# Kernel tuning notes

Hardware: AMD Instinct MI355X
Metric: run time of the kernel (lower is better)

The kernel has to match this reference:

```python
import jax, jax.numpy as jnp
import numpy as np

N_HEADS = 32
N_KV_HEADS = 8
HEAD_DIM = 128
GROUP = N_HEADS // N_KV_HEADS  # 4
MAX_SEQ_LEN = 4096
DIM = 3072
NEG_BIG = 1.0e9


def setup_inputs() -> dict:
    key = jax.random.key(0)
    ks = jax.random.split(key, 8)
    B, T = 1, 2048
    return {
        "x": jax.random.normal(ks[0], (B, T, DIM), dtype=jnp.float32),
        "freqs_cos": jax.random.uniform(ks[1], (T, HEAD_DIM // 2), dtype=jnp.float32),
        "freqs_sin": jax.random.uniform(ks[2], (T, HEAD_DIM // 2), dtype=jnp.float32),
        "input_pos": jnp.arange(T, dtype=jnp.int32),
        "wq": jax.random.normal(ks[3], (N_HEADS * HEAD_DIM, DIM), dtype=jnp.float32) * 0.02,
        "wk": jax.random.normal(ks[4], (N_KV_HEADS * HEAD_DIM, DIM), dtype=jnp.float32) * 0.02,
        "wv": jax.random.normal(ks[5], (N_KV_HEADS * HEAD_DIM, DIM), dtype=jnp.float32) * 0.02,
        "wo": jax.random.normal(ks[6], (DIM, N_HEADS * HEAD_DIM), dtype=jnp.float32) * 0.02,
        "k_cache": jnp.zeros((1, N_KV_HEADS, MAX_SEQ_LEN, HEAD_DIM), dtype=jnp.float32),
        "v_cache": jnp.zeros((1, N_KV_HEADS, MAX_SEQ_LEN, HEAD_DIM), dtype=jnp.float32),
    }


def _rotate_half(x):
    half = x.shape[-1] // 2
    return jnp.concatenate([-x[..., half:], x[..., :half]], axis=-1)


def _apply_rope(q, k, freqs_cos, freqs_sin):
    # freqs: [T, D/2] -> [1, T, 1, D] (tiled x2, matching torch repeat on last dim)
    fc = jnp.concatenate([freqs_cos, freqs_cos], axis=-1)[None, :, None, :]
    fs = jnp.concatenate([freqs_sin, freqs_sin], axis=-1)[None, :, None, :]
    qf = q.astype(jnp.float32)
    kf = k.astype(jnp.float32)
    q_out = qf * fc + _rotate_half(qf) * fs
    k_out = kf * fc + _rotate_half(kf) * fs
    return q_out.astype(q.dtype), k_out.astype(k.dtype)


def reference(x, freqs_cos, freqs_sin, input_pos, wq, wk, wv, wo, k_cache, v_cache):
    B, T, _ = x.shape
    # QKV projections
    q = (x @ wq.T).reshape(B, T, N_HEADS, HEAD_DIM)
    k = (x @ wk.T).reshape(B, T, N_KV_HEADS, HEAD_DIM)
    v = (x @ wv.T).reshape(B, T, N_KV_HEADS, HEAD_DIM)
    # split-half RoPE (computed in fp32)
    q, k = _apply_rope(q, k, freqs_cos, freqs_sin)
    # StaticKVCache.update: scatter [B,H,T,D] into [1,H,S,D] cache at input_pos (dim 2)
    kc = k_cache.at[:, :, input_pos].set(k.transpose(0, 2, 1, 3))
    vc = v_cache.at[:, :, input_pos].set(v.transpose(0, 2, 1, 3))
    # MetalSDPA: additive causal mask over full cache length
    S = kc.shape[2]
    k_pos = jnp.arange(S)
    valid = jnp.clip(input_pos[:, None] - k_pos[None, :] + 1, 0, 1)  # [T, S]
    mask = (valid.astype(q.dtype) - 1.0) * NEG_BIG
    # GQA attention: group q heads per kv head
    qg = q.transpose(0, 2, 1, 3).reshape(B, N_KV_HEADS, GROUP, T, HEAD_DIM)
    scale = 1.0 / jnp.sqrt(jnp.asarray(HEAD_DIM, dtype=q.dtype))
    scores = jnp.einsum('bhgtd,bhsd->bhgts', qg, kc) * scale + mask  # [B,Hk,G,T,S]
    attn = jax.nn.softmax(scores, axis=-1)
    y = jnp.einsum('bhgts,bhsd->bhgtd', attn, vc)
    y = y.reshape(B, N_HEADS, T, HEAD_DIM).transpose(0, 2, 1, 3).reshape(B, T, N_HEADS * HEAD_DIM)
    return y @ wo.T
```

## Files before the change

kernel.cpp:

```cpp
#include <hip/hip_runtime.h>

typedef __attribute__((ext_vector_type(8))) short bf16x8;
typedef __attribute__((ext_vector_type(4))) float f32x4;

#define T_SEQ   2048
#define DIM     3072
#define NQH     32
#define NKVH    8
#define HD      128
#define QDIM    4096
#define KVDIM   1024
#define QKVDIM  6144

#define AS1 __attribute__((address_space(1)))
#define AS3 __attribute__((address_space(3)))

static __device__ __forceinline__ unsigned short f2bf(float f) {
  unsigned u = __float_as_uint(f);
  u += 0x7FFFu + ((u >> 16) & 1u);
  return (unsigned short)(u >> 16);
}
static __device__ __forceinline__ float bf2f(unsigned short h) {
  return __uint_as_float(((unsigned)h) << 16);
}

static __device__ __forceinline__ void gload_lds16(const unsigned short* g, unsigned short* l) {
  __builtin_amdgcn_global_load_lds((AS1 void*)(g), (AS3 void*)(l), 16, 0, 0);
}

__global__ void cvt_f32_bf16(const float* __restrict__ src, unsigned short* __restrict__ dst, int n4) {
  int i = blockIdx.x * blockDim.x + threadIdx.x;
  if (i >= n4) return;
  float4 v = reinterpret_cast<const float4*>(src)[i];
  ushort4 o;
  o.x = f2bf(v.x); o.y = f2bf(v.y); o.z = f2bf(v.z); o.w = f2bf(v.w);
  reinterpret_cast<ushort4*>(dst)[i] = o;
}

template<int OUTBF>
__global__ __launch_bounds__(256) void gemm_bt(
    const unsigned short* __restrict__ A, const unsigned short* __restrict__ B,
    float* __restrict__ Cf, unsigned short* __restrict__ Cb,
    int M, int N, int K) {
  __shared__ unsigned short la[128 * 64];
  __shared__ unsigned short lb[128 * 64];
  const int nbx = N >> 7;
  const int q8 = gridDim.x >> 3;
  int bid = blockIdx.x;
  bid = (bid & 7) * q8 + (bid >> 3);
  const int bx = bid % nbx, by = bid / nbx;
  const int tid = threadIdx.x;
  const int ln = tid & 63;
  const int wave = tid >> 6;
  const int lr = ln & 15, lg = ln >> 4;
  const int wr = wave >> 1, wc = wave & 1;
  const int rowA0 = by << 7, rowB0 = bx << 7;

  f32x4 acc[4][4] = {};

  const int ktn = K >> 6;
  for (int kt = 0; kt < ktn; kt++) {
    __syncthreads();
#pragma unroll
    for (int it = 0; it < 4; it++) {
      int ci = it * 256 + tid;
      int r = ci >> 3, cpos = ci & 7;
      int c = cpos ^ (r & 7);
      const unsigned short* gA = A + (size_t)(rowA0 + r) * K + kt * 64 + c * 8;
      const unsigned short* gB = B + (size_t)(rowB0 + r) * K + kt * 64 + c * 8;
      gload_lds16(gA, &la[ci * 8]);
      gload_lds16(gB, &lb[ci * 8]);
    }
    __syncthreads();
#pragma unroll
    for (int kk = 0; kk < 2; kk++) {
      bf16x8 af[4], bfr[4];
#pragma unroll
      for (int mi = 0; mi < 4; mi++) {
        int r = wr * 64 + mi * 16 + lr;
        int p = (kk * 4 + lg) ^ (r & 7);
        af[mi] = *reinterpret_cast<const bf16x8*>(&la[r * 64 + p * 8]);
      }
#pragma unroll
      for (int ni = 0; ni < 4; ni++) {
        int r = wc * 64 + ni * 16 + lr;
        int p = (kk * 4 + lg) ^ (r & 7);
        bfr[ni] = *reinterpret_cast<const bf16x8*>(&lb[r * 64 + p * 8]);
      }
#pragma unroll
      for (int mi = 0; mi < 4; mi++)
#pragma unroll
        for (int ni = 0; ni < 4; ni++)
          acc[mi][ni] = __builtin_amdgcn_mfma_f32_16x16x32_bf16(af[mi], bfr[ni], acc[mi][ni], 0, 0, 0);
    }
  }
#pragma unroll
  for (int mi = 0; mi < 4; mi++)
#pragma unroll
    for (int ni = 0; ni < 4; ni++)
#pragma unroll
      for (int j = 0; j < 4; j++) {
        int r = rowA0 + wr * 64 + mi * 16 + lg * 4 + j;
        int cc = rowB0 + wc * 64 + ni * 16 + lr;
        if (OUTBF) Cb[(size_t)r * N + cc] = f2bf(acc[mi][ni][j]);
        else       Cf[(size_t)r * N + cc] = acc[mi][ni][j];
      }
}

__global__ void rope_repack(const unsigned short* __restrict__ qkv,
                            const float* __restrict__ fc, const float* __restrict__ fs,
                            unsigned short* __restrict__ qo, unsigned short* __restrict__ ko) {
  int idx = blockIdx.x * blockDim.x + threadIdx.x;
  int d = idx & 63;
  int hh = (idx >> 6) % 40;
  int t = idx / 2560;
  const unsigned short* src = qkv + (size_t)t * QKVDIM + hh * 128;
  float x0 = bf2f(src[d]);
  float x1 = bf2f(src[d + 64]);
  float c = fc[t * 64 + d], s = fs[t * 64 + d];
  float o0 = x0 * c - x1 * s;
  float o1 = x1 * c + x0 * s;
  if (hh < 32) {
    unsigned short* dst = qo + (size_t)t * QDIM + hh * 128;
    dst[d] = f2bf(o0); dst[d + 64] = f2bf(o1);
  } else {
    unsigned short* dst = ko + (size_t)t * KVDIM + (hh - 32) * 128;
    dst[d] = f2bf(o0); dst[d + 64] = f2bf(o1);
  }
}

__global__ void vtrans(const unsigned short* __restrict__ qkv, unsigned short* __restrict__ vt) {
  __shared__ unsigned short tile[64][68];
  int tb = blockIdx.x * 64, cb = blockIdx.y * 64;
  int tid = threadIdx.x;
#pragma unroll
  for (int i = 0; i < 16; i++) {
    int e = i * 256 + tid;
    int tl = e >> 6, cl = e & 63;
    tile[tl][cl] = qkv[(size_t)(tb + tl) * QKVDIM + 5120 + cb + cl];
  }
  __syncthreads();
#pragma unroll
  for (int i = 0; i < 16; i++) {
    int e = i * 256 + tid;
    int cl = e >> 6, tl = e & 63;
    vt[(size_t)(cb + cl) * T_SEQ + tb + tl] = tile[tl][cl];
  }
}

__global__ __launch_bounds__(256) void attn_fwd(
    const unsigned short* __restrict__ q, const unsigned short* __restrict__ k,
    const unsigned short* __restrict__ vt, unsigned short* __restrict__ y) {
  __shared__ unsigned short k_lds[32 * 128];
  __shared__ unsigned short v_lds[128 * 32];
  __shared__ unsigned short p_lds[4][16 * 40];
  __shared__ float a_lds[4][16];
  const int tid = threadIdx.x;
  const int ln = tid & 63;
  const int wave = tid >> 6;
  const int lr = ln & 15, lg = ln >> 4;

  const int kh = blockIdx.x & 7;
  const int i = blockIdx.x >> 3;
  const int qh = i & 3;
  const int j = i >> 2;
  const int qt = (j & 1) ? (31 - (j >> 1)) : (j >> 1);
  const int h = kh * 4 + qh;

  const int qr0 = qt * 64 + wave * 16;
  const int qrow = qr0 + lr;
  const float SL2E = 0.08838834764831845f * 1.44269504088896f;
  const float NEGINF = -__builtin_inff();

  bf16x8 qf[4];
  const unsigned short* qb = q + (size_t)qrow * QDIM + h * HD + lg * 8;
#pragma unroll
  for (int dc = 0; dc < 4; dc++) qf[dc] = *reinterpret_cast<const bf16x8*>(qb + dc * 32);

  f32x4 acc[8] = {};
  float m = NEGINF, lsum = 0.f;

  const int ntiles = (qt * 64 + 95) >> 5;
  for (int st = 0; st < ntiles; st++) {
    const int sb = st * 32;

    bf16x8 kr[2], vr[2];
#pragma unroll
    for (int it = 0; it < 2; it++) {
      int id = tid + it * 256;
      int r = id >> 4, c = id & 15;
      kr[it] = *reinterpret_cast<const bf16x8*>(k + (size_t)(sb + r) * KVDIM + kh * HD + c * 8);
      int d = id >> 2, cv = id & 3;
      vr[it] = *reinterpret_cast<const bf16x8*>(vt + (size_t)(kh * HD + d) * T_SEQ + sb + cv * 8);
    }
    __syncthreads();
#pragma unroll
    for (int it = 0; it < 2; it++) {
      int id = tid + it * 256;
      int r = id >> 4, c = id & 15;
      *reinterpret_cast<bf16x8*>(&k_lds[r * 128 + (c ^ (r & 7)) * 8]) = kr[it];
      int d = id >> 2, cv = id & 3;
      *reinterpret_cast<bf16x8*>(&v_lds[d * 32 + (cv ^ ((d >> 1) & 3)) * 8]) = vr[it];
    }
    __syncthreads();

    if (sb <= qr0 + 15) {
      f32x4 s0t = {0.f, 0.f, 0.f, 0.f}, s1t = {0.f, 0.f, 0.f, 0.f};
#pragma unroll
      for (int dc = 0; dc < 4; dc++) {
        int c = lg + dc * 4;
        int p = c ^ (lr & 7);
        bf16x8 a0 = *reinterpret_cast<const bf16x8*>(&k_lds[lr * 128 + p * 8]);
        bf16x8 a1 = *reinterpret_cast<const bf16x8*>(&k_lds[(lr + 16) * 128 + p * 8]);
        s0t = __builtin_amdgcn_mfma_f32_16x16x32_bf16(a0, qf[dc], s0t, 0, 0, 0);
        s1t = __builtin_amdgcn_mfma_f32_16x16x32_bf16(a1, qf[dc], s1t, 0, 0, 0);
      }

      float vv[8];
      if (sb + 31 <= qr0) {
#pragma unroll
        for (int jj = 0; jj < 4; jj++) { vv[jj] = s0t[jj]; vv[jj + 4] = s1t[jj]; }
      } else {
        const int base0 = sb + lg * 4;
#pragma unroll
        for (int jj = 0; jj < 4; jj++) {
          vv[jj]     = (base0 + jj      <= qrow) ? s0t[jj] : NEGINF;
          vv[jj + 4] = (base0 + jj + 16 <= qrow) ? s1t[jj] : NEGINF;
        }
      }

      float mx = fmaxf(fmaxf(fmaxf(vv[0], vv[1]), fmaxf(vv[2], vv[3])),
                       fmaxf(fmaxf(vv[4], vv[5]), fmaxf(vv[6], vv[7])));
      mx = fmaxf(mx, __shfl_xor(mx, 16));
      mx = fmaxf(mx, __shfl_xor(mx, 32));

      const bool doresc = __any(mx > m + 60.0f);
      const float mn = doresc ? fmaxf(m, mx) : m;

      float p[8], ps = 0.f;
#pragma unroll
      for (int ii = 0; ii < 8; ii++) { p[ii] = exp2f((vv[ii] - mn) * SL2E); ps += p[ii]; }
      ps += __shfl_xor(ps, 16);
      ps += __shfl_xor(ps, 32);

      ushort4 pw0, pw1;
      pw0.x = f2bf(p[0]); pw0.y = f2bf(p[1]); pw0.z = f2bf(p[2]); pw0.w = f2bf(p[3]);
      pw1.x = f2bf(p[4]); pw1.y = f2bf(p[5]); pw1.z = f2bf(p[6]); pw1.w = f2bf(p[7]);
      *reinterpret_cast<ushort4*>(&p_lds[wave][lr * 40 + lg * 4])      = pw0;
      *reinterpret_cast<ushort4*>(&p_lds[wave][lr * 40 + 16 + lg * 4]) = pw1;

      if (doresc) {
        const float alpha = exp2f((m - mn) * SL2E);
        lsum = lsum * alpha + ps;
        m = mn;
        a_lds[wave][lr] = alpha;
        asm volatile("s_waitcnt lgkmcnt(0)" ::: "memory");
        float4 a4 = *reinterpret_cast<const float4*>(&a_lds[wave][lg * 4]);
#pragma unroll
        for (int dc2 = 0; dc2 < 8; dc2++) {
          acc[dc2][0] *= a4.x; acc[dc2][1] *= a4.y;
          acc[dc2][2] *= a4.z; acc[dc2][3] *= a4.w;
        }
      } else {
        lsum += ps;
        asm volatile("s_waitcnt lgkmcnt(0)" ::: "memory");
      }

      bf16x8 pa = *reinterpret_cast<const bf16x8*>(&p_lds[wave][lr * 40 + lg * 8]);
#pragma unroll
      for (int dc2 = 0; dc2 < 8; dc2++) {
        int d = dc2 * 16 + lr;
        int p2 = lg ^ ((d >> 1) & 3);
        bf16x8 bv = *reinterpret_cast<const bf16x8*>(&v_lds[d * 32 + p2 * 8]);
        acc[dc2] = __builtin_amdgcn_mfma_f32_16x16x32_bf16(pa, bv, acc[dc2], 0, 0, 0);
      }
    }
  }

  a_lds[wave][lr] = 1.0f / lsum;
  asm volatile("s_waitcnt lgkmcnt(0)" ::: "memory");
  float4 l4 = *reinterpret_cast<const float4*>(&a_lds[wave][lg * 4]);
  float li[4] = {l4.x, l4.y, l4.z, l4.w};
#pragma unroll
  for (int jj = 0; jj < 4; jj++) {
    int r = qr0 + lg * 4 + jj;
#pragma unroll
    for (int dc2 = 0; dc2 < 8; dc2++)
      y[(size_t)r * QDIM + h * HD + dc2 * 16 + lr] = f2bf(acc[dc2][jj] * li[jj]);
  }
}

extern "C" void kernel_launch(void* const* d_in, const int* in_sizes, int n_in,
                              void* d_out, int out_size, void* d_ws, size_t ws_size,
                              hipStream_t stream) {
  (void)in_sizes; (void)n_in; (void)out_size; (void)ws_size;
  const float* x    = (const float*)d_in[0];
  const float* fcos = (const float*)d_in[1];
  const float* fsin = (const float*)d_in[2];
  const float* wq   = (const float*)d_in[4];
  const float* wk   = (const float*)d_in[5];
  const float* wv   = (const float*)d_in[6];
  const float* wo   = (const float*)d_in[7];
  float* out = (float*)d_out;
  char* ws = (char*)d_ws;

  unsigned short* x_bf    = (unsigned short*)(ws);
  unsigned short* wqkv_bf = (unsigned short*)(ws + 12582912);
  unsigned short* qkv_bf  = (unsigned short*)(ws + 50331648);
  unsigned short* q_bf    = (unsigned short*)(ws);
  unsigned short* k_bf    = (unsigned short*)(ws + 16777216);
  unsigned short* vt_bf   = (unsigned short*)(ws + 20971520);
  unsigned short* y_bf    = (unsigned short*)(ws + 25165824);
  unsigned short* wo_bf   = (unsigned short*)(ws + 50331648);

  cvt_f32_bf16<<<6144,  256, 0, stream>>>(x,  x_bf,               2048 * 3072 / 4);
  cvt_f32_bf16<<<12288, 256, 0, stream>>>(wq, wqkv_bf,            4096 * 3072 / 4);
  cvt_f32_bf16<<<3072,  256, 0, stream>>>(wk, wqkv_bf + 4096*3072, 1024 * 3072 / 4);
  cvt_f32_bf16<<<3072,  256, 0, stream>>>(wv, wqkv_bf + 5120*3072, 1024 * 3072 / 4);
  gemm_bt<1><<<768, 256, 0, stream>>>(x_bf, wqkv_bf, nullptr, qkv_bf, 2048, 6144, 3072);

  rope_repack<<<20480, 256, 0, stream>>>(qkv_bf, fcos, fsin, q_bf, k_bf);
  vtrans<<<dim3(32, 16), 256, 0, stream>>>(qkv_bf, vt_bf);

  cvt_f32_bf16<<<12288, 256, 0, stream>>>(wo, wo_bf, 3072 * 4096 / 4);
  attn_fwd<<<1024, 256, 0, stream>>>(q_bf, k_bf, vt_bf, y_bf);
  gemm_bt<0><<<384, 256, 0, stream>>>(y_bf, wo_bf, out, nullptr, 2048, 3072, 4096);
}
```

Baseline: 326.9 us.

## Double-buffer K/V tiles in attention with register prefetch and MFMA priority

The attention kernel now double-buffers its K and V LDS tiles. Each iteration loads the next tile into registers before computing on the current one and writes it to the other buffer afterwards, so there is one barrier per tile instead of two. It also raises wave priority around the MFMA loops and changes the query-tile ordering from interleaved heavy/light to longest-first. LDS use doubles, which may reduce occupancy, and the prefetch registers add pressure.

```diff
diff --git a/kernel.cpp b/kernel.cpp
--- a/kernel.cpp
+++ b/kernel.cpp
@@ -151,8 +151,8 @@
 __global__ __launch_bounds__(256) void attn_fwd(
     const unsigned short* __restrict__ q, const unsigned short* __restrict__ k,
     const unsigned short* __restrict__ vt, unsigned short* __restrict__ y) {
-  __shared__ unsigned short k_lds[32 * 128];
-  __shared__ unsigned short v_lds[128 * 32];
+  __shared__ unsigned short k_lds[2][32 * 128];
+  __shared__ unsigned short v_lds[2][128 * 32];
   __shared__ unsigned short p_lds[4][16 * 40];
   __shared__ float a_lds[4][16];
   const int tid = threadIdx.x;
@@ -163,8 +163,7 @@
   const int kh = blockIdx.x & 7;
   const int i = blockIdx.x >> 3;
   const int qh = i & 3;
-  const int j = i >> 2;
-  const int qt = (j & 1) ? (31 - (j >> 1)) : (j >> 1);
+  const int qt = 31 - (i >> 2);
   const int h = kh * 4 + qh;
 
   const int qr0 = qt * 64 + wave * 16;
@@ -180,41 +179,52 @@
   f32x4 acc[8] = {};
   float m = NEGINF, lsum = 0.f;
 
+  const int krow0 = tid >> 4,      kcol0 = tid & 15;
+  const int krow1 = 16 + krow0;
+  const int vrow0 = tid >> 2,      vcol0 = tid & 3;
+  const int vrow1 = 64 + vrow0;
+
   const int ntiles = (qt * 64 + 95) >> 5;
+
+  {
+    bf16x8 kr0 = *reinterpret_cast<const bf16x8*>(k + (size_t)krow0 * KVDIM + kh * HD + kcol0 * 8);
+    bf16x8 kr1 = *reinterpret_cast<const bf16x8*>(k + (size_t)krow1 * KVDIM + kh * HD + kcol0 * 8);
+    bf16x8 vr0 = *reinterpret_cast<const bf16x8*>(vt + (size_t)(kh * HD + vrow0) * T_SEQ + vcol0 * 8);
+    bf16x8 vr1 = *reinterpret_cast<const bf16x8*>(vt + (size_t)(kh * HD + vrow1) * T_SEQ + vcol0 * 8);
+    *reinterpret_cast<bf16x8*>(&k_lds[0][krow0 * 128 + (kcol0 ^ (krow0 & 7)) * 8]) = kr0;
+    *reinterpret_cast<bf16x8*>(&k_lds[0][krow1 * 128 + (kcol0 ^ (krow1 & 7)) * 8]) = kr1;
+    *reinterpret_cast<bf16x8*>(&v_lds[0][vrow0 * 32 + (vcol0 ^ ((vrow0 >> 1) & 3)) * 8]) = vr0;
+    *reinterpret_cast<bf16x8*>(&v_lds[0][vrow1 * 32 + (vcol0 ^ ((vrow1 >> 1) & 3)) * 8]) = vr1;
+  }
+  __syncthreads();
+
   for (int st = 0; st < ntiles; st++) {
     const int sb = st * 32;
-
-    bf16x8 kr[2], vr[2];
-#pragma unroll
-    for (int it = 0; it < 2; it++) {
-      int id = tid + it * 256;
-      int r = id >> 4, c = id & 15;
-      kr[it] = *reinterpret_cast<const bf16x8*>(k + (size_t)(sb + r) * KVDIM + kh * HD + c * 8);
-      int d = id >> 2, cv = id & 3;
-      vr[it] = *reinterpret_cast<const bf16x8*>(vt + (size_t)(kh * HD + d) * T_SEQ + sb + cv * 8);
-    }
-    __syncthreads();
-#pragma unroll
-    for (int it = 0; it < 2; it++) {
-      int id = tid + it * 256;
-      int r = id >> 4, c = id & 15;
-      *reinterpret_cast<bf16x8*>(&k_lds[r * 128 + (c ^ (r & 7)) * 8]) = kr[it];
-      int d = id >> 2, cv = id & 3;
-      *reinterpret_cast<bf16x8*>(&v_lds[d * 32 + (cv ^ ((d >> 1) & 3)) * 8]) = vr[it];
-    }
-    __syncthreads();
+    const int cur = st & 1;
+    const bool more = (st + 1 < ntiles);
+
+    bf16x8 kr0, kr1, vr0, vr1;
+    if (more) {
+      const int sb1 = sb + 32;
+      kr0 = *reinterpret_cast<const bf16x8*>(k + (size_t)(sb1 + krow0) * KVDIM + kh * HD + kcol0 * 8);
+      kr1 = *reinterpret_cast<const bf16x8*>(k + (size_t)(sb1 + krow1) * KVDIM + kh * HD + kcol0 * 8);
+      vr0 = *reinterpret_cast<const bf16x8*>(vt + (size_t)(kh * HD + vrow0) * T_SEQ + sb1 + vcol0 * 8);
+      vr1 = *reinterpret_cast<const bf16x8*>(vt + (size_t)(kh * HD + vrow1) * T_SEQ + sb1 + vcol0 * 8);
+    }
 
     if (sb <= qr0 + 15) {
       f32x4 s0t = {0.f, 0.f, 0.f, 0.f}, s1t = {0.f, 0.f, 0.f, 0.f};
+      __builtin_amdgcn_s_setprio(1);
 #pragma unroll
       for (int dc = 0; dc < 4; dc++) {
         int c = lg + dc * 4;
         int p = c ^ (lr & 7);
-        bf16x8 a0 = *reinterpret_cast<const bf16x8*>(&k_lds[lr * 128 + p * 8]);
-        bf16x8 a1 = *reinterpret_cast<const bf16x8*>(&k_lds[(lr + 16) * 128 + p * 8]);
+        bf16x8 a0 = *reinterpret_cast<const bf16x8*>(&k_lds[cur][lr * 128 + p * 8]);
+        bf16x8 a1 = *reinterpret_cast<const bf16x8*>(&k_lds[cur][(lr + 16) * 128 + p * 8]);
         s0t = __builtin_amdgcn_mfma_f32_16x16x32_bf16(a0, qf[dc], s0t, 0, 0, 0);
         s1t = __builtin_amdgcn_mfma_f32_16x16x32_bf16(a1, qf[dc], s1t, 0, 0, 0);
       }
+      __builtin_amdgcn_s_setprio(0);
 
       float vv[8];
       if (sb + 31 <= qr0) {
@@ -267,13 +277,24 @@
       }
 
       bf16x8 pa = *reinterpret_cast<const bf16x8*>(&p_lds[wave][lr * 40 + lg * 8]);
+      __builtin_amdgcn_s_setprio(1);
 #pragma unroll
       for (int dc2 = 0; dc2 < 8; dc2++) {
         int d = dc2 * 16 + lr;
         int p2 = lg ^ ((d >> 1) & 3);
-        bf16x8 bv = *reinterpret_cast<const bf16x8*>(&v_lds[d * 32 + p2 * 8]);
+        bf16x8 bv = *reinterpret_cast<const bf16x8*>(&v_lds[cur][d * 32 + p2 * 8]);
         acc[dc2] = __builtin_amdgcn_mfma_f32_16x16x32_bf16(pa, bv, acc[dc2], 0, 0, 0);
       }
+      __builtin_amdgcn_s_setprio(0);
+    }
+
+    if (more) {
+      const int nxt = cur ^ 1;
+      *reinterpret_cast<bf16x8*>(&k_lds[nxt][krow0 * 128 + (kcol0 ^ (krow0 & 7)) * 8]) = kr0;
+      *reinterpret_cast<bf16x8*>(&k_lds[nxt][krow1 * 128 + (kcol0 ^ (krow1 & 7)) * 8]) = kr1;
+      *reinterpret_cast<bf16x8*>(&v_lds[nxt][vrow0 * 32 + (vcol0 ^ ((vrow0 >> 1) & 3)) * 8]) = vr0;
+      *reinterpret_cast<bf16x8*>(&v_lds[nxt][vrow1 * 32 + (vcol0 ^ ((vrow1 >> 1) & 3)) * 8]) = vr1;
+      __syncthreads();
     }
   }
 
```

Result: no change. 329.6 us (+0.8%).
